# Optimization experiments

Hardware: AMD Instinct MI355X
Metric: run time of the kernel (lower is better)

The kernel has to match this reference:

```python
import jax, jax.numpy as jnp
import numpy as np

V, C, H, T, B, D = 32000, 768, 12, 1024, 2, 4
HID = C // 2
FF = 4 * C
HD = C // H


def _ln(x, s, b):
    m = jnp.mean(x, axis=-1, keepdims=True)
    v = jnp.mean((x - m) ** 2, axis=-1, keepdims=True)
    return (x - m) * jax.lax.rsqrt(v + 1e-5) * s + b


def setup_inputs() -> dict:
    key = jax.random.key(0)
    ks = jax.random.split(key, 12)
    nrm = lambda k, shp: 0.02 * jax.random.normal(k, shp, dtype=jnp.float32)
    return {
        "idx": jax.random.randint(ks[0], (B, T), 0, V),
        "tok_emb": nrm(ks[1], (V, C)),
        "pos_emb": nrm(ks[2], (T, C)),
        "r_w1": nrm(ks[3], (C, HID)), "r_b1": jnp.zeros((HID,), jnp.float32),
        "r_w2": nrm(ks[4], (HID, D)), "r_b2": jnp.zeros((D,), jnp.float32),
        "ln1_s": jnp.ones((C,), jnp.float32), "ln1_b": jnp.zeros((C,), jnp.float32),
        "qkv_w": nrm(ks[5], (C, 3 * C)),
        "proj_w": nrm(ks[6], (C, C)), "proj_b": jnp.zeros((C,), jnp.float32),
        "ln2_s": jnp.ones((C,), jnp.float32), "ln2_b": jnp.zeros((C,), jnp.float32),
        "f_w1": nrm(ks[7], (C, FF)), "f_b1": jnp.zeros((FF,), jnp.float32),
        "f_w2": nrm(ks[8], (FF, C)), "f_b2": jnp.zeros((C,), jnp.float32),
        "lnf_s": jnp.ones((C,), jnp.float32), "lnf_b": jnp.zeros((C,), jnp.float32),
        "head_w": nrm(ks[9], (V, C)),  # torch Linear weight [out, in]
    }


def reference(idx, tok_emb, pos_emb, r_w1, r_b1, r_w2, r_b2,
              ln1_s, ln1_b, qkv_w, proj_w, proj_b, ln2_s, ln2_b,
              f_w1, f_b1, f_w2, f_b2, lnf_s, lnf_b, head_w):
    # embeddings
    x = tok_emb[idx] + pos_emb[None, :, :]  # [B,T,C]

    # depth router (eval mode: hard one-hot argmax, k=1)
    rh = jax.nn.relu(x @ r_w1 + r_b1)
    r_logits = rh @ r_w2 + r_b2  # [B,T,D]
    w = jax.nn.one_hot(jnp.argmax(r_logits, axis=-1), D, dtype=x.dtype)  # [B,T,D]

    causal = jnp.tril(jnp.ones((T, T), dtype=bool))
    scale = 1.0 / np.sqrt(HD).astype(np.float32)

    def block(z):
        # pre-norm attention
        y = _ln(z, ln1_s, ln1_b)
        qkv = y @ qkv_w  # [B,T,3C]
        q, k, v = jnp.split(qkv, 3, axis=-1)
        q = q.reshape(B, T, H, HD)
        k = k.reshape(B, T, H, HD)
        v = v.reshape(B, T, H, HD)
        att = jnp.einsum('bqhd,bkhd->bhqk', q, k) * scale
        att = jnp.where(causal, att, -jnp.inf)
        att = jax.nn.softmax(att, axis=-1)
        o = jnp.einsum('bhqk,bkhd->bqhd', att, v).reshape(B, T, C)
        z = z + (o @ proj_w + proj_b)
        # pre-norm FFN (dropout inactive in eval)
        y2 = _ln(z, ln2_s, ln2_b)
        ff = jax.nn.gelu(y2 @ f_w1 + f_b1, approximate=False) @ f_w2 + f_b2
        return z + ff

    # depth-d output = block applied (d+1) times; accumulate with router weight
    out = jnp.zeros_like(x)
    h = x
    for d in range(D):
        h = block(h)
        out = out + w[:, :, d:d + 1] * h

    xf = _ln(out, lnf_s, lnf_b)
    logits = xf @ head_w.T  # [B,T,V]
    return logits
```

## Files before the change

### kernel.cpp

```cpp
#include <hip/hip_runtime.h>
#include <hip/hip_bf16.h>

typedef unsigned short u16;
typedef __bf16 bf16x8 __attribute__((ext_vector_type(8)));
typedef float f32x4 __attribute__((ext_vector_type(4)));

#define DEVINL __device__ __forceinline__

DEVINL u16 f2b(float f){
  unsigned u = __float_as_uint(f);
  u += 0x7FFFu + ((u >> 16) & 1u);
  return (u16)(u >> 16);
}
DEVINL float b2f(u16 b){ return __uint_as_float(((unsigned)b) << 16); }

DEVINL void gload16(const void* g, void* l){
  __builtin_amdgcn_global_load_lds(
      (const __attribute__((address_space(1))) unsigned*)g,
      (__attribute__((address_space(3))) unsigned*)l, 16, 0, 0);
}

__global__ __launch_bounds__(256) void k_embed(const int* __restrict__ idx,
    const float* __restrict__ tok, const float* __restrict__ pos, float* __restrict__ h){
  int r = blockIdx.x, t = threadIdx.x;
  int token = idx[r];
  const float* tr = tok + (long)token * 768;
  const float* pr = pos + (long)(r & 1023) * 768;
  float* hr = h + (long)r * 768;
  hr[t]       = tr[t]       + pr[t];
  hr[t + 256] = tr[t + 256] + pr[t + 256];
  hr[t + 512] = tr[t + 512] + pr[t + 512];
}

__global__ __launch_bounds__(256) void k_ln(const float* __restrict__ X,
    const float* __restrict__ s, const float* __restrict__ b, u16* __restrict__ Y){
  int r = blockIdx.x, t = threadIdx.x;
  const float* x = X + (long)r * 768;
  float v0 = x[t], v1 = x[t + 256], v2 = x[t + 512];
  float sum = v0 + v1 + v2;
  __shared__ float tmp[4];
  #pragma unroll
  for (int o = 32; o; o >>= 1) sum += __shfl_xor(sum, o);
  int wave = t >> 6;
  if ((t & 63) == 0) tmp[wave] = sum;
  __syncthreads();
  sum = tmp[0] + tmp[1] + tmp[2] + tmp[3];
  float m = sum * (1.f / 768.f);
  float d0 = v0 - m, d1 = v1 - m, d2 = v2 - m;
  float sq = d0 * d0 + d1 * d1 + d2 * d2;
  #pragma unroll
  for (int o = 32; o; o >>= 1) sq += __shfl_xor(sq, o);
  __syncthreads();
  if ((t & 63) == 0) tmp[wave] = sq;
  __syncthreads();
  sq = tmp[0] + tmp[1] + tmp[2] + tmp[3];
  float rs = rsqrtf(sq * (1.f / 768.f) + 1e-5f);
  u16* y = Y + (long)r * 768;
  y[t]       = f2b(d0 * rs * s[t]       + b[t]);
  y[t + 256] = f2b(d1 * rs * s[t + 256] + b[t + 256]);
  y[t + 512] = f2b(d2 * rs * s[t + 512] + b[t + 512]);
}

__global__ __launch_bounds__(256) void k_wt(const float* __restrict__ W, u16* __restrict__ Wt,
                                            int K, int N){
  __shared__ float tile[32][33];
  int kb = blockIdx.x * 32, nb = blockIdx.y * 32;
  int tx = threadIdx.x & 31, ty = threadIdx.x >> 5;
  #pragma unroll
  for (int i = 0; i < 32; i += 8) tile[ty + i][tx] = W[(long)(kb + ty + i) * N + nb + tx];
  __syncthreads();
  #pragma unroll
  for (int i = 0; i < 32; i += 8) Wt[(long)(nb + ty + i) * K + kb + tx] = f2b(tile[tx][ty + i]);
}

__global__ __launch_bounds__(256) void k_conv(const float* __restrict__ W, u16* __restrict__ O, long n4){
  long i = (long)blockIdx.x * 256 + threadIdx.x;
  if (i >= n4) return;
  float4 v = ((const float4*)W)[i];
  unsigned lo = (unsigned)f2b(v.x) | ((unsigned)f2b(v.y) << 16);
  unsigned hi = (unsigned)f2b(v.z) | ((unsigned)f2b(v.w) << 16);
  ((uint2*)O)[i] = make_uint2(lo, hi);
}

__global__ __launch_bounds__(256) void k_r1(const float* __restrict__ A, const float* __restrict__ B,
    const float* __restrict__ bias, float* __restrict__ C){
  __shared__ float As[64][17];
  __shared__ float Bs[16][65];
  int r0 = blockIdx.x * 64, c0 = blockIdx.y * 64;
  int t = threadIdx.x;
  int tx = t & 15, ty = t >> 4;
  float acc[4][4] = {};
  for (int k0 = 0; k0 < 768; k0 += 16){
    #pragma unroll
    for (int i = 0; i < 4; i++){ int e = i * 256 + t; As[e >> 4][e & 15] = A[(long)(r0 + (e >> 4)) * 768 + k0 + (e & 15)]; }
    #pragma unroll
    for (int i = 0; i < 4; i++){ int e = i * 256 + t; Bs[e >> 6][e & 63] = B[(long)(k0 + (e >> 6)) * 384 + c0 + (e & 63)]; }
    __syncthreads();
    #pragma unroll
    for (int kk = 0; kk < 16; kk++){
      float a[4], bb[4];
      #pragma unroll
      for (int i = 0; i < 4; i++) a[i] = As[ty * 4 + i][kk];
      #pragma unroll
      for (int j = 0; j < 4; j++) bb[j] = Bs[kk][tx * 4 + j];
      #pragma unroll
      for (int i = 0; i < 4; i++)
        #pragma unroll
        for (int j = 0; j < 4; j++) acc[i][j] += a[i] * bb[j];
    }
    __syncthreads();
  }
  #pragma unroll
  for (int i = 0; i < 4; i++)
    #pragma unroll
    for (int j = 0; j < 4; j++){
      int rr = r0 + ty * 4 + i, cc = c0 + tx * 4 + j;
      float v = acc[i][j] + bias[cc];
      C[(long)rr * 384 + cc] = v > 0.f ? v : 0.f;
    }
}

__global__ __launch_bounds__(64) void k_r2(const float* __restrict__ rh, const float* __restrict__ w2,
    const float* __restrict__ b2, int* __restrict__ sel){
  int tkn = blockIdx.x, l = threadIdx.x;
  float s0 = 0, s1 = 0, s2 = 0, s3 = 0;
  const float* r = rh + (long)tkn * 384;
  for (int k = l; k < 384; k += 64){
    float rv = r[k];
    float4 w = ((const float4*)w2)[k];
    s0 += rv * w.x; s1 += rv * w.y; s2 += rv * w.z; s3 += rv * w.w;
  }
  #pragma unroll
  for (int o = 32; o; o >>= 1){
    s0 += __shfl_xor(s0, o); s1 += __shfl_xor(s1, o);
    s2 += __shfl_xor(s2, o); s3 += __shfl_xor(s3, o);
  }
  if (l == 0){
    float v[4] = { s0 + b2[0], s1 + b2[1], s2 + b2[2], s3 + b2[3] };
    int am = 0; float bv = v[0];
    #pragma unroll
    for (int j = 1; j < 4; j++) if (v[j] > bv){ bv = v[j]; am = j; }
    sel[tkn] = am;
  }
}

__global__ __launch_bounds__(256) void k_attn(
    const u16* __restrict__ qkv, const u16* __restrict__ Vt, u16* __restrict__ o){
  __shared__ __align__(16) u16 Klds[64][64];
  __shared__ __align__(16) u16 Vlds[64][64];
  __shared__ __align__(16) u16 Plds[4][16][72];
  int qt = blockIdx.x, bh = blockIdx.y;
  int b = bh / 12, hh = bh % 12;
  int t = threadIdx.x, w = t >> 6, lane = t & 63;
  int lr = lane & 15, koct = lane >> 4;
  int q0 = qt * 64 + w * 16;
  const u16* Qrow = qkv + ((long)(b * 1024 + q0 + lr)) * 2304 + hh * 64;
  bf16x8 qf[2];
  qf[0] = __builtin_bit_cast(bf16x8, *(const uint4*)&Qrow[koct * 8]);
  qf[1] = __builtin_bit_cast(bf16x8, *(const uint4*)&Qrow[32 + koct * 8]);
  f32x4 oacc[4] = {};
  float m_run[4], l_run[4];
  #pragma unroll
  for (int r = 0; r < 4; r++){ m_run[r] = -1e30f; l_run[r] = 0.f; }
  int srow8 = lane >> 3, scolb = (lane & 7) * 16;
  const char* Kbase = (const char*)(qkv + (long)b * 1024 * 2304 + 768 + hh * 64);
  const char* Vbase = (const char*)(Vt + (long)bh * 64 * 1024);
  for (int kvt = 0; kvt <= qt; ++kvt){
    #pragma unroll
    for (int i = 0; i < 2; i++){
      int row = w * 16 + i * 8 + srow8;
      int sb = scolb ^ ((row & 7) << 4);
      gload16(Kbase + (long)(kvt * 64 + row) * 4608 + sb, &Klds[w * 16 + i * 8][0]);
    }
    #pragma unroll
    for (int i = 0; i < 2; i++){
      int row = w * 16 + i * 8 + srow8;
      int sb = scolb ^ ((row & 7) << 4);
      gload16(Vbase + (long)row * 2048 + kvt * 128 + sb, &Vlds[w * 16 + i * 8][0]);
    }
    __syncthreads();
    f32x4 sacc[4] = {};
    #pragma unroll
    for (int j = 0; j < 4; j++){
      #pragma unroll
      for (int f = 0; f < 2; f++){
        int row = 16 * j + lr;
        bf16x8 kf = __builtin_bit_cast(bf16x8, *(const uint4*)(
            (const char*)&Klds[0][0] + row * 128 + ((64 * f + koct * 16) ^ ((row & 7) << 4))));
        sacc[j] = __builtin_amdgcn_mfma_f32_16x16x32_bf16(qf[f], kf, sacc[j], 0, 0, 0);
      }
    }
    bool diag = (kvt == qt);
    float p[4][4];
    #pragma unroll
    for (int r = 0; r < 4; r++){
      int qg = q0 + 4 * koct + r;
      float vj[4];
      #pragma unroll
      for (int j = 0; j < 4; j++){
        int kvg = kvt * 64 + 16 * j + lr;
        float v = sacc[j][r] * 0.125f;
        vj[j] = (!diag || kvg <= qg) ? v : -1e30f;
      }
      float mx = fmaxf(fmaxf(vj[0], vj[1]), fmaxf(vj[2], vj[3]));
      #pragma unroll
      for (int s = 1; s < 16; s <<= 1) mx = fmaxf(mx, __shfl_xor(mx, s));
      float mn = fmaxf(m_run[r], mx);
      float sc = __expf(m_run[r] - mn);
      float rs = 0.f;
      #pragma unroll
      for (int j = 0; j < 4; j++){ p[j][r] = __expf(vj[j] - mn); rs += p[j][r]; }
      #pragma unroll
      for (int s = 1; s < 16; s <<= 1) rs += __shfl_xor(rs, s);
      l_run[r] = l_run[r] * sc + rs;
      m_run[r] = mn;
      #pragma unroll
      for (int j = 0; j < 4; j++) oacc[j][r] *= sc;
    }
    #pragma unroll
    for (int r = 0; r < 4; r++)
      #pragma unroll
      for (int j = 0; j < 4; j++)
        Plds[w][4 * koct + r][16 * j + lr] = f2b(p[j][r]);
    bf16x8 pf[2];
    pf[0] = __builtin_bit_cast(bf16x8, *(const uint4*)&Plds[w][lr][koct * 8]);
    pf[1] = __builtin_bit_cast(bf16x8, *(const uint4*)&Plds[w][lr][32 + koct * 8]);
    #pragma unroll
    for (int j = 0; j < 4; j++){
      #pragma unroll
      for (int f = 0; f < 2; f++){
        int row = 16 * j + lr;
        bf16x8 vf = __builtin_bit_cast(bf16x8, *(const uint4*)(
            (const char*)&Vlds[0][0] + row * 128 + ((64 * f + koct * 16) ^ ((row & 7) << 4))));
        oacc[j] = __builtin_amdgcn_mfma_f32_16x16x32_bf16(pf[f], vf, oacc[j], 0, 0, 0);
      }
    }
    __syncthreads();
  }
  float inv[4];
  #pragma unroll
  for (int r = 0; r < 4; r++) inv[r] = 1.f / l_run[r];
  #pragma unroll
  for (int j = 0; j < 4; j++){
    #pragma unroll
    for (int r = 0; r < 4; r++){
      int tq = b * 1024 + q0 + 4 * koct + r;
      o[(long)tq * 768 + hh * 64 + 16 * j + lr] = f2b(oacc[j][r] * inv[r]);
    }
  }
}

__global__ __launch_bounds__(256) void k_redln(const float* __restrict__ P, int nparts,
    const float* __restrict__ bias, const float* __restrict__ resid, float* __restrict__ outh,
    const float* __restrict__ ls, const float* __restrict__ lb, u16* __restrict__ Y,
    const int* __restrict__ sel, float* __restrict__ outb, int d){
  int r = blockIdx.x, t = threadIdx.x;
  float v0, v1, v2;
  {
    float a0 = bias[t]       + resid[(long)r * 768 + t];
    float a1 = bias[t + 256] + resid[(long)r * 768 + t + 256];
    float a2 = bias[t + 512] + resid[(long)r * 768 + t + 512];
    for (int p = 0; p < nparts; p++){
      const float* pr = P + ((long)p * 2048 + r) * 768;
      a0 += pr[t]; a1 += pr[t + 256]; a2 += pr[t + 512];
    }
    v0 = a0; v1 = a1; v2 = a2;
  }
  float* hr = outh + (long)r * 768;
  hr[t] = v0; hr[t + 256] = v1; hr[t + 512] = v2;
  if (sel && sel[r] == d){
    float* orow = outb + (long)r * 768;
    orow[t] = v0; orow[t + 256] = v1; orow[t + 512] = v2;
  }
  float sum = v0 + v1 + v2;
  __shared__ float tmp[4];
  #pragma unroll
  for (int o = 32; o; o >>= 1) sum += __shfl_xor(sum, o);
  int wave = t >> 6;
  if ((t & 63) == 0) tmp[wave] = sum;
  __syncthreads();
  sum = tmp[0] + tmp[1] + tmp[2] + tmp[3];
  float m = sum * (1.f / 768.f);
  float d0 = v0 - m, d1 = v1 - m, d2 = v2 - m;
  float sq = d0 * d0 + d1 * d1 + d2 * d2;
  #pragma unroll
  for (int o = 32; o; o >>= 1) sq += __shfl_xor(sq, o);
  __syncthreads();
  if ((t & 63) == 0) tmp[wave] = sq;
  __syncthreads();
  sq = tmp[0] + tmp[1] + tmp[2] + tmp[3];
  float rs = rsqrtf(sq * (1.f / 768.f) + 1e-5f);
  u16* y = Y + (long)r * 768;
  y[t]       = f2b(d0 * rs * ls[t]       + lb[t]);
  y[t + 256] = f2b(d1 * rs * ls[t + 256] + lb[t + 256]);
  y[t + 512] = f2b(d2 * rs * ls[t + 512] + lb[t + 512]);
}

__global__ __launch_bounds__(64) void k_gemm1(
    const u16* __restrict__ A, int lda, long s1A, long s2A,
    const u16* __restrict__ B, int ldb, long s1B, long s2B,
    void* Cv, int ldc, long s1C, long s2C,
    const float* __restrict__ bias,
    const float* __restrict__ resid, int ldr,
    int K, int zdiv, int ksegK, int flags, u16* __restrict__ vtbuf){
  __shared__ __align__(16) u16 As[2][64][32];
  __shared__ __align__(16) u16 Bs[2][64][32];
  int lane = threadIdx.x;
  int bx = blockIdx.x, by = blockIdx.y, bz = blockIdx.z;
  if (flags & 16){
    int nx = gridDim.x, nwg = nx * gridDim.y;
    int lin = by * nx + bx;
    int q = nwg >> 3;
    int nl = (lin & 7) * q + (lin >> 3);
    bx = nl % nx; by = nl / nx;
  }
  int row0 = bx * 64, col0 = by * 64;
  int zq = bz / zdiv, zr = bz % zdiv;
  A += zq * s2A + (long)zr * s1A;
  B += zq * s2B + (long)zr * s1B;
  long coff = zq * s2C + (long)zr * s1C;
  int kstart = 0, Klim = K;
  if (ksegK > 0){ kstart = bz * ksegK; Klim = kstart + ksegK; }
  f32x4 acc[4][4] = {};
  int lr = lane & 15, lk = (lane >> 4) * 8;
  int srow = lane >> 2, scol = (lane & 3) * 16;
  int nt = (Klim - kstart) >> 5;
  auto STAGE = [&](int buf, int k0){
    #pragma unroll
    for (int i = 0; i < 4; i++)
      gload16((const char*)&A[(long)(row0 + i * 16 + srow) * lda + k0] + scol, &As[buf][i * 16][0]);
    #pragma unroll
    for (int i = 0; i < 4; i++)
      gload16((const char*)&B[(long)(col0 + i * 16 + srow) * ldb + k0] + scol, &Bs[buf][i * 16][0]);
  };
  STAGE(0, kstart);
  int cur = 0;
  for (int t = 0; t < nt; t++){
    if (t + 1 < nt){
      STAGE(cur ^ 1, kstart + ((t + 1) << 5));
      asm volatile("s_waitcnt vmcnt(8)" ::: "memory");
    } else {
      asm volatile("s_waitcnt vmcnt(0)" ::: "memory");
    }
    __builtin_amdgcn_sched_barrier(0);
    bf16x8 af[4], bb[4];
    #pragma unroll
    for (int i = 0; i < 4; i++)
      af[i] = __builtin_bit_cast(bf16x8, *(const uint4*)&As[cur][i * 16 + lr][lk]);
    #pragma unroll
    for (int j = 0; j < 4; j++)
      bb[j] = __builtin_bit_cast(bf16x8, *(const uint4*)&Bs[cur][j * 16 + lr][lk]);
    #pragma unroll
    for (int i = 0; i < 4; i++)
      #pragma unroll
      for (int j = 0; j < 4; j++)
        acc[i][j] = __builtin_amdgcn_mfma_f32_16x16x32_bf16(af[i], bb[j], acc[i][j], 0, 0, 0);
    __builtin_amdgcn_sched_barrier(0);
    cur ^= 1;
  }
  bool vmode = (vtbuf != nullptr) && (col0 >= 1536);
  if (vmode){
    #pragma unroll
    for (int i = 0; i < 4; i++){
      int rbase = row0 + i * 16 + ((lane >> 4) << 2);
      int b = rbase >> 10, tt = rbase & 1023;
      #pragma unroll
      for (int j = 0; j < 4; j++){
        int cc = col0 + j * 16 + lr;
        int hh = (cc - 1536) >> 6, dd = (cc - 1536) & 63;
        unsigned lo = (unsigned)f2b(acc[i][j][0]) | ((unsigned)f2b(acc[i][j][1]) << 16);
        unsigned hi = (unsigned)f2b(acc[i][j][2]) | ((unsigned)f2b(acc[i][j][3]) << 16);
        *(uint2*)&vtbuf[((long)(b * 12 + hh) * 64 + dd) * 1024 + tt] = make_uint2(lo, hi);
      }
    }
    return;
  }
  #pragma unroll
  for (int i = 0; i < 4; i++){
    int rbase = row0 + i * 16 + ((lane >> 4) << 2);
    #pragma unroll
    for (int j = 0; j < 4; j++){
      int cc = col0 + j * 16 + lr;
      #pragma unroll
      for (int q = 0; q < 4; q++){
        int rr = rbase + q;
        float v = acc[i][j][q];
        if (bias) v += bias[cc];
        if (flags & 2) v = 0.5f * v * (1.f + erff(v * 0.70710678118654752f));
        if (resid) v += resid[(long)rr * ldr + cc];
        if (flags & 1) ((u16*)Cv)[coff + (long)rr * ldc + cc] = f2b(v);
        else           ((float*)Cv)[coff + (long)rr * ldc + cc] = v;
      }
    }
  }
}

template<int BM, int BN>
__global__ __launch_bounds__(256) void k_gemm(
    const u16* __restrict__ A, int lda,
    const u16* __restrict__ B, int ldb,
    void* Cv, int ldc,
    int K, int flags){
  constexpr int FM = BM / 32, FN = BN / 32;
  __shared__ __align__(16) u16 As[BM][32];
  __shared__ __align__(16) u16 Bs[BN][32];
  int t = threadIdx.x;
  int wave = t >> 6, lane = t & 63;
  int wm = wave >> 1, wn = wave & 1;
  int bx = blockIdx.x, by = blockIdx.y;
  if (flags & 16){
    int nx = gridDim.x, nwg = nx * gridDim.y;
    int lin = by * nx + bx;
    int q = nwg >> 3;
    int nl = (lin & 7) * q + (lin >> 3);
    bx = nl % nx; by = nl / nx;
  }
  int row0 = bx * BM, col0 = by * BN;
  f32x4 acc[FM][FN] = {};
  int lr = lane & 15, lk = (lane >> 4) * 8;
  int lrow = lane >> 2, lcolb = (lane & 3) * 16;
  for (int k0 = 0; k0 < K; k0 += 32){
    #pragma unroll
    for (int i = 0; i < BM / 64; i++){
      int r = i * 64 + wave * 16;
      gload16((const char*)&A[(long)(row0 + r + lrow) * lda + k0] + lcolb, &As[r][0]);
    }
    #pragma unroll
    for (int i = 0; i < BN / 64; i++){
      int r = i * 64 + wave * 16;
      gload16((const char*)&B[(long)(col0 + r + lrow) * ldb + k0] + lcolb, &Bs[r][0]);
    }
    __syncthreads();
    bf16x8 af[FM], bfr[FN];
    #pragma unroll
    for (int i = 0; i < FM; i++)
      af[i] = __builtin_bit_cast(bf16x8, *(const uint4*)&As[wm * FM * 16 + i * 16 + lr][lk]);
    #pragma unroll
    for (int j = 0; j < FN; j++)
      bfr[j] = __builtin_bit_cast(bf16x8, *(const uint4*)&Bs[wn * FN * 16 + j * 16 + lr][lk]);
    #pragma unroll
    for (int i = 0; i < FM; i++)
      #pragma unroll
      for (int j = 0; j < FN; j++)
        acc[i][j] = __builtin_amdgcn_mfma_f32_16x16x32_bf16(af[i], bfr[j], acc[i][j], 0, 0, 0);
    __syncthreads();
  }
  #pragma unroll
  for (int i = 0; i < FM; i++){
    int rbase = row0 + wm * FM * 16 + i * 16 + (lane >> 4) * 4;
    #pragma unroll
    for (int j = 0; j < FN; j++){
      int cc = col0 + wn * FN * 16 + j * 16 + lr;
      #pragma unroll
      for (int q = 0; q < 4; q++){
        int rr = rbase + q;
        ((float*)Cv)[(long)rr * ldc + cc] = acc[i][j][q];
      }
    }
  }
}

extern "C" void kernel_launch(void* const* d_in, const int* in_sizes, int n_in,
                              void* d_out, int out_size, void* d_ws, size_t ws_size,
                              hipStream_t stream){
  const int*   idx    = (const int*)d_in[0];
  const float* tok    = (const float*)d_in[1];
  const float* pos    = (const float*)d_in[2];
  const float* r_w1   = (const float*)d_in[3];
  const float* r_b1   = (const float*)d_in[4];
  const float* r_w2   = (const float*)d_in[5];
  const float* r_b2   = (const float*)d_in[6];
  const float* ln1_s  = (const float*)d_in[7];
  const float* ln1_b  = (const float*)d_in[8];
  const float* qkv_w  = (const float*)d_in[9];
  const float* proj_w = (const float*)d_in[10];
  const float* proj_b = (const float*)d_in[11];
  const float* ln2_s  = (const float*)d_in[12];
  const float* ln2_b  = (const float*)d_in[13];
  const float* f_w1   = (const float*)d_in[14];
  const float* f_b1   = (const float*)d_in[15];
  const float* f_w2   = (const float*)d_in[16];
  const float* f_b2   = (const float*)d_in[17];
  const float* lnf_s  = (const float*)d_in[18];
  const float* lnf_b  = (const float*)d_in[19];
  const float* head_w = (const float*)d_in[20];
  float* logits = (float*)d_out;

  char* w = (char*)d_ws;
  size_t off = 0;
  auto alloc = [&](size_t bytes)->char*{ char* p = w + off; off += (bytes + 255) & ~(size_t)255; return p; };
  u16*   wqT  = (u16*)  alloc(2304ull * 768 * 2);
  u16*   wpT  = (u16*)  alloc(768ull * 768 * 2);
  u16*   wf1T = (u16*)  alloc(3072ull * 768 * 2);
  u16*   wf2T = (u16*)  alloc(768ull * 3072 * 2);
  u16*   whd  = (u16*)  alloc(32000ull * 768 * 2);
  float* h    = (float*)alloc(2048ull * 768 * 4);
  float* outb = (float*)alloc(2048ull * 768 * 4);
  u16*   y    = (u16*)  alloc(2048ull * 768 * 2);
  u16*   qkv  = (u16*)  alloc(2048ull * 2304 * 2);
  u16*   o    = (u16*)  alloc(2048ull * 768 * 2);
  u16*   ffh  = (u16*)  alloc(2048ull * 3072 * 2);
  u16*   Vt   = (u16*)  alloc(24ull * 64 * 1024 * 2);
  float* rh   = (float*)alloc(2048ull * 384 * 4);
  int*   sel  = (int*)  alloc(2048 * 4);
  float* Sf   = (float*)alloc(4ull * 2048 * 768 * 4);
  (void)in_sizes; (void)n_in; (void)out_size; (void)ws_size;

  dim3 b256(256), b64(64);
  k_wt<<<dim3(24, 72), b256, 0, stream>>>(qkv_w,  wqT,  768, 2304);
  k_wt<<<dim3(24, 24), b256, 0, stream>>>(proj_w, wpT,  768, 768);
  k_wt<<<dim3(24, 96), b256, 0, stream>>>(f_w1,   wf1T, 768, 3072);
  k_wt<<<dim3(96, 24), b256, 0, stream>>>(f_w2,   wf2T, 3072, 768);
  k_conv<<<24000, b256, 0, stream>>>(head_w, whd, 6144000);
  k_embed<<<2048, b256, 0, stream>>>(idx, tok, pos, h);
  k_r1<<<dim3(32, 6), b256, 0, stream>>>(h, r_w1, r_b1, rh);
  k_r2<<<2048, b64, 0, stream>>>(rh, r_w2, r_b2, sel);
  k_ln<<<2048, b256, 0, stream>>>(h, ln1_s, ln1_b, y);

  for (int d = 0; d < 4; ++d){
    k_gemm1<<<dim3(32, 36), b64, 0, stream>>>(
        y, 768, 0, 0, wqT, 768, 0, 0, qkv, 2304, 0, 0,
        nullptr, nullptr, 0, 768, 12, 0, 1 | 16, Vt);
    k_attn<<<dim3(16, 24), b256, 0, stream>>>(qkv, Vt, o);
    k_gemm1<<<dim3(32, 12, 4), b64, 0, stream>>>(
        o, 768, 0, 0, wpT, 768, 0, 0, Sf, 768, 2048ll * 768, 0,
        nullptr, nullptr, 0, 768, 12, 192, 16, nullptr);
    k_redln<<<2048, b256, 0, stream>>>(Sf, 4, proj_b, h, h, ln2_s, ln2_b, y,
                                       nullptr, nullptr, 0);
    k_gemm1<<<dim3(32, 48), b64, 0, stream>>>(
        y, 768, 0, 0, wf1T, 768, 0, 0, ffh, 3072, 0, 0,
        f_b1, nullptr, 0, 768, 12, 0, 1 | 2 | 16, nullptr);
    k_gemm1<<<dim3(32, 12, 4), b64, 0, stream>>>(
        ffh, 3072, 0, 0, wf2T, 3072, 0, 0, Sf, 768, 2048ll * 768, 0,
        nullptr, nullptr, 0, 3072, 12, 768, 16, nullptr);
    k_redln<<<2048, b256, 0, stream>>>(Sf, 4, f_b2, h, h, ln1_s, ln1_b, y,
                                       sel, outb, d);
  }
  k_ln<<<2048, b256, 0, stream>>>(outb, lnf_s, lnf_b, y);
  k_gemm<128, 128><<<dim3(16, 250), b256, 0, stream>>>(
      y, 768, whd, 768, logits, 32000, 768, 16);
}
```

Before: 935.0 us.

## Replace LM-head GEMM with double-buffered swizzled 256x256 tile kernel

The generic 128x128 head GEMM is replaced by a dedicated 512-thread kernel with 256x256 tiles and K-step 64. It double-buffers LDS with async global-to-LDS loads, XOR-swizzles LDS rows to avoid bank conflicts, and raises wave priority around the MFMA blocks so loads overlap compute. Separately, the attention projection split-K is reduced from 4 to 2 splits, which cuts the reduction traffic at the cost of fewer workgroups. The large LDS footprint (128KB) and register use may limit occupancy.

```diff
diff --git a/kernel.cpp b/kernel.cpp
--- a/kernel.cpp
+++ b/kernel.cpp
@@ -395,67 +395,92 @@
   }
 }
 
-template<int BM, int BN>
-__global__ __launch_bounds__(256) void k_gemm(
-    const u16* __restrict__ A, int lda,
-    const u16* __restrict__ B, int ldb,
-    void* Cv, int ldc,
-    int K, int flags){
-  constexpr int FM = BM / 32, FN = BN / 32;
-  __shared__ __align__(16) u16 As[BM][32];
-  __shared__ __align__(16) u16 Bs[BN][32];
-  int t = threadIdx.x;
-  int wave = t >> 6, lane = t & 63;
-  int wm = wave >> 1, wn = wave & 1;
+__global__ __launch_bounds__(512, 2) void k_head(
+    const u16* __restrict__ A, const u16* __restrict__ B, float* __restrict__ C){
+  __shared__ __align__(16) u16 As[2][256][64];
+  __shared__ __align__(16) u16 Bs[2][256][64];
+  const int lda = 768, ldb = 768, ldc = 32000;
+  int t = threadIdx.x, w = t >> 6, lane = t & 63;
+  int wm = w >> 2, wn = w & 3;
   int bx = blockIdx.x, by = blockIdx.y;
-  if (flags & 16){
+  {
     int nx = gridDim.x, nwg = nx * gridDim.y;
     int lin = by * nx + bx;
     int q = nwg >> 3;
     int nl = (lin & 7) * q + (lin >> 3);
     bx = nl % nx; by = nl / nx;
   }
-  int row0 = bx * BM, col0 = by * BN;
-  f32x4 acc[FM][FN] = {};
-  int lr = lane & 15, lk = (lane >> 4) * 8;
-  int lrow = lane >> 2, lcolb = (lane & 3) * 16;
-  for (int k0 = 0; k0 < K; k0 += 32){
-    #pragma unroll
-    for (int i = 0; i < BM / 64; i++){
-      int r = i * 64 + wave * 16;
-      gload16((const char*)&A[(long)(row0 + r + lrow) * lda + k0] + lcolb, &As[r][0]);
-    }
-    #pragma unroll
-    for (int i = 0; i < BN / 64; i++){
-      int r = i * 64 + wave * 16;
-      gload16((const char*)&B[(long)(col0 + r + lrow) * ldb + k0] + lcolb, &Bs[r][0]);
-    }
+  long row0 = (long)bx * 256, col0 = (long)by * 256;
+  int srow = lane >> 3;
+  int scolb = (lane & 7) * 16;
+  int lr = lane & 15, koct = lane >> 4;
+  f32x4 acc[8][4] = {};
+  const int nt = 12;
+  auto STAGE_A = [&](int buf, int k0){
+    #pragma unroll
+    for (int g = 0; g < 4; g++){
+      int row = g * 64 + w * 8 + srow;
+      gload16((const char*)&A[(row0 + row) * lda + k0] + (scolb ^ ((row & 7) << 4)),
+              &As[buf][g * 64 + w * 8][0]);
+    }
+  };
+  auto STAGE_B = [&](int buf, int k0){
+    #pragma unroll
+    for (int g = 0; g < 4; g++){
+      int row = g * 64 + w * 8 + srow;
+      gload16((const char*)&B[(col0 + row) * ldb + k0] + (scolb ^ ((row & 7) << 4)),
+              &Bs[buf][g * 64 + w * 8][0]);
+    }
+  };
+  STAGE_A(0, 0);
+  STAGE_B(0, 0);
+  int cur = 0;
+  for (int kt = 0; kt < nt; kt++){
+    bool more = kt + 1 < nt;
+    if (more){
+      STAGE_A(cur ^ 1, (kt + 1) * 64);
+      asm volatile("s_waitcnt vmcnt(4)" ::: "memory");
+    } else {
+      asm volatile("s_waitcnt vmcnt(0)" ::: "memory");
+    }
+    __builtin_amdgcn_sched_barrier(0);
     __syncthreads();
-    bf16x8 af[FM], bfr[FN];
-    #pragma unroll
-    for (int i = 0; i < FM; i++)
-      af[i] = __builtin_bit_cast(bf16x8, *(const uint4*)&As[wm * FM * 16 + i * 16 + lr][lk]);
-    #pragma unroll
-    for (int j = 0; j < FN; j++)
-      bfr[j] = __builtin_bit_cast(bf16x8, *(const uint4*)&Bs[wn * FN * 16 + j * 16 + lr][lk]);
-    #pragma unroll
-    for (int i = 0; i < FM; i++)
-      #pragma unroll
-      for (int j = 0; j < FN; j++)
-        acc[i][j] = __builtin_amdgcn_mfma_f32_16x16x32_bf16(af[i], bfr[j], acc[i][j], 0, 0, 0);
+    #pragma unroll
+    for (int s = 0; s < 2; s++){
+      bf16x8 af[8], bfr[4];
+      #pragma unroll
+      for (int i = 0; i < 8; i++){
+        int row = wm * 128 + i * 16 + lr;
+        af[i] = __builtin_bit_cast(bf16x8, *(const uint4*)(
+            (const char*)&As[cur][0][0] + row * 128 + ((s * 64 + koct * 16) ^ ((row & 7) << 4))));
+      }
+      #pragma unroll
+      for (int j = 0; j < 4; j++){
+        int row = wn * 64 + j * 16 + lr;
+        bfr[j] = __builtin_bit_cast(bf16x8, *(const uint4*)(
+            (const char*)&Bs[cur][0][0] + row * 128 + ((s * 64 + koct * 16) ^ ((row & 7) << 4))));
+      }
+      if (s == 0 && more) STAGE_B(cur ^ 1, (kt + 1) * 64);
+      __builtin_amdgcn_s_setprio(1);
+      #pragma unroll
+      for (int i = 0; i < 8; i++)
+        #pragma unroll
+        for (int j = 0; j < 4; j++)
+          acc[i][j] = __builtin_amdgcn_mfma_f32_16x16x32_bf16(af[i], bfr[j], acc[i][j], 0, 0, 0);
+      __builtin_amdgcn_s_setprio(0);
+    }
     __syncthreads();
-  }
-  #pragma unroll
-  for (int i = 0; i < FM; i++){
-    int rbase = row0 + wm * FM * 16 + i * 16 + (lane >> 4) * 4;
-    #pragma unroll
-    for (int j = 0; j < FN; j++){
-      int cc = col0 + wn * FN * 16 + j * 16 + lr;
-      #pragma unroll
-      for (int q = 0; q < 4; q++){
-        int rr = rbase + q;
-        ((float*)Cv)[(long)rr * ldc + cc] = acc[i][j][q];
-      }
+    cur ^= 1;
+  }
+  #pragma unroll
+  for (int i = 0; i < 8; i++){
+    long rbase = row0 + wm * 128 + i * 16 + koct * 4;
+    #pragma unroll
+    for (int j = 0; j < 4; j++){
+      long cc = col0 + wn * 64 + j * 16 + lr;
+      #pragma unroll
+      for (int q = 0; q < 4; q++)
+        C[(rbase + q) * ldc + cc] = acc[i][j][q];
     }
   }
 }
@@ -522,10 +547,10 @@
         y, 768, 0, 0, wqT, 768, 0, 0, qkv, 2304, 0, 0,
         nullptr, nullptr, 0, 768, 12, 0, 1 | 16, Vt);
     k_attn<<<dim3(16, 24), b256, 0, stream>>>(qkv, Vt, o);
-    k_gemm1<<<dim3(32, 12, 4), b64, 0, stream>>>(
+    k_gemm1<<<dim3(32, 12, 2), b64, 0, stream>>>(
         o, 768, 0, 0, wpT, 768, 0, 0, Sf, 768, 2048ll * 768, 0,
-        nullptr, nullptr, 0, 768, 12, 192, 16, nullptr);
-    k_redln<<<2048, b256, 0, stream>>>(Sf, 4, proj_b, h, h, ln2_s, ln2_b, y,
+        nullptr, nullptr, 0, 768, 12, 384, 16, nullptr);
+    k_redln<<<2048, b256, 0, stream>>>(Sf, 2, proj_b, h, h, ln2_s, ln2_b, y,
                                        nullptr, nullptr, 0);
     k_gemm1<<<dim3(32, 48), b64, 0, stream>>>(
         y, 768, 0, 0, wf1T, 768, 0, 0, ffh, 3072, 0, 0,
@@ -537,6 +562,5 @@
                                        sel, outb, d);
   }
   k_ln<<<2048, b256, 0, stream>>>(outb, lnf_s, lnf_b, y);
-  k_gemm<128, 128><<<dim3(16, 250), b256, 0, stream>>>(
-      y, 768, whd, 768, logits, 32000, 768, 16);
-}
+  k_head<<<dim3(8, 125), dim3(512), 0, stream>>>(y, whd, logits);
+}
```

Result: faster. 895.8 us (-4.2%).
